# Performance work log

Hardware: AMD Instinct MI355X
Metric: run time of the kernel (lower is better)

The kernel has to match this reference:

```python
import jax, jax.numpy as jnp
import numpy as np

NUM_HEADS = 16
LN_EPS = 1e-5


def _layernorm(x, g, b):
    mu = jnp.mean(x, axis=-1, keepdims=True)
    var = jnp.mean(jnp.square(x - mu), axis=-1, keepdims=True)
    return (x - mu) * jax.lax.rsqrt(var + LN_EPS) * g + b


def setup_inputs() -> dict:
    key = jax.random.key(0)
    ks = jax.random.split(key, 8)
    B, S, D = 4, 2048, 1024
    s = 0.02  # small init so softmax/layernorm stay well-conditioned
    return {
        "x": jax.random.normal(ks[0], (B, S, D), jnp.float32),
        "wq_w": jax.random.normal(ks[1], (D, D), jnp.float32) * s,
        "wq_b": jnp.zeros((D,), jnp.float32),
        "wk_w": jax.random.normal(ks[2], (D, D), jnp.float32) * s,
        "wk_b": jnp.zeros((D,), jnp.float32),
        "wv_w": jax.random.normal(ks[3], (D, D), jnp.float32) * s,
        "wv_b": jnp.zeros((D,), jnp.float32),
        "ln1_g": jnp.ones((D,), jnp.float32),
        "ln1_b": jnp.zeros((D,), jnp.float32),
        "lin1_w": jax.random.normal(ks[4], (D, D), jnp.float32) * s,
        "lin1_b": jnp.zeros((D,), jnp.float32),
        "ln2_g": jnp.ones((D,), jnp.float32),
        "ln2_b": jnp.zeros((D,), jnp.float32),
    }


def reference(x, wq_w, wq_b, wk_w, wk_b, wv_w, wv_b,
              ln1_g, ln1_b, lin1_w, lin1_b, ln2_g, ln2_b):
    B, S, D = x.shape
    H = NUM_HEADS
    dh = D // H

    def proj(w, b):
        # torch Linear: x @ w.T + b ; split heads -> [B,H,S,dh]
        return (x @ w.T + b).reshape(B, S, H, dh).transpose(0, 2, 1, 3)

    q, k, v = proj(wq_w, wq_b), proj(wk_w, wk_b), proj(wv_w, wv_b)

    scores = jnp.einsum("bhqd,bhkd->bhqk", q, k) / jnp.sqrt(jnp.float32(dh))
    causal = jnp.tril(jnp.ones((S, S), jnp.bool_))  # True = attend
    scores = jnp.where(causal[None, None], scores, -jnp.inf)
    probs = jax.nn.softmax(scores, axis=-1)
    attn = jnp.einsum("bhqk,bhkd->bhqd", probs, v)
    attn = attn.transpose(0, 2, 1, 3).reshape(B, S, D)

    h = _layernorm(x + attn, ln1_g, ln1_b)
    h = _layernorm(h + (h @ lin1_w.T + lin1_b), ln2_g, ln2_b)
    return h
```

## Files before the change

### kernel.cpp

```cpp
#include <hip/hip_runtime.h>
#include <math.h>

#define B_  4
#define S_  2048
#define D_  1024
#define H_  16
#define DH_ 64
#define M_  (B_*S_)

typedef unsigned short ushort_t;
typedef __attribute__((ext_vector_type(8))) __bf16 bf16x8;
typedef __attribute__((ext_vector_type(4))) float f32x4;
typedef __attribute__((ext_vector_type(8))) unsigned short us8;
typedef __attribute__((ext_vector_type(4))) unsigned short us4;

__device__ __forceinline__ ushort_t f2bf(float f) {
    unsigned int u = __float_as_uint(f);
    u = (u + 0x7fffu + ((u >> 16) & 1u)) >> 16;
    return (ushort_t)u;
}
__device__ __forceinline__ float bf2f(ushort_t u) {
    return __uint_as_float(((unsigned int)u) << 16);
}

#define GLD16(gp, lp) __builtin_amdgcn_global_load_lds( \
    (const __attribute__((address_space(1))) void*)(gp), \
    (__attribute__((address_space(3))) void*)(lp), 16, 0, 0)

#define WAIT_VM0()   __builtin_amdgcn_s_waitcnt(0x0F70)
#define WAIT_VM4()   __builtin_amdgcn_s_waitcnt(0x0F74)
#define WAIT_VM8()   __builtin_amdgcn_s_waitcnt(0x0F78)
#define MEMFENCE()   asm volatile("" ::: "memory")
#define BAR()        do { MEMFENCE(); __builtin_amdgcn_s_barrier(); MEMFENCE(); } while (0)

__global__ __launch_bounds__(256)
void cvt_all(const float* __restrict__ x,
             const float* __restrict__ w0, const float* __restrict__ w1,
             const float* __restrict__ w2, const float* __restrict__ w3,
             ushort_t* __restrict__ xd, ushort_t* __restrict__ wd)
{
    const int bid = blockIdx.x;
    const float* s;
    ushort_t* d;
    int i;
    if (bid < 4096) {
        s = x; d = xd; i = bid * 2048 + threadIdx.x * 8;
    } else {
        const int k = (bid - 4096) >> 9;
        const int r = (bid - 4096) & 511;
        s = (k == 0) ? w0 : (k == 1) ? w1 : (k == 2) ? w2 : w3;
        d = wd + (size_t)k * (D_ * D_);
        i = r * 2048 + threadIdx.x * 8;
    }
    float4 a = *(const float4*)(s + i);
    float4 b = *(const float4*)(s + i + 4);
    us8 r8;
    r8[0] = f2bf(a.x); r8[1] = f2bf(a.y); r8[2] = f2bf(a.z); r8[3] = f2bf(a.w);
    r8[4] = f2bf(b.x); r8[5] = f2bf(b.y); r8[6] = f2bf(b.z); r8[7] = f2bf(b.w);
    *(us8*)(d + i) = r8;
}

__global__ __launch_bounds__(256)
void gemm_mfma(const ushort_t* __restrict__ A, const ushort_t* __restrict__ Bw,
               const float* __restrict__ bias0, const float* __restrict__ bias1,
               const float* __restrict__ bias2,
               ushort_t* __restrict__ Yb, ushort_t* __restrict__ Qo,
               ushort_t* __restrict__ Ko, ushort_t* __restrict__ Vo,
               int K, int mode)
{
    __shared__ __align__(16) ushort_t As[3][128 * 32];
    __shared__ __align__(16) ushort_t Bs[3][128 * 32];
    const int t = threadIdx.x;
    const int lane = t & 63, wave = t >> 6;
    const int wm = wave >> 1, wn = wave & 1;
    const int m0 = blockIdx.x * 128, n0 = blockIdx.y * 128;
    const int quad = lane >> 4, l15 = lane & 15;

    const int ch0 = wave * 2, ch1 = wave * 2 + 1;
    const int srow = lane >> 2;
    const int scol = 8 * ((lane & 3) ^ (srow & 3));
    const ushort_t* Ap0 = A  + (size_t)(m0 + ch0 * 16 + srow) * K + scol;
    const ushort_t* Ap1 = A  + (size_t)(m0 + ch1 * 16 + srow) * K + scol;
    const ushort_t* Bp0 = Bw + (size_t)(n0 + ch0 * 16 + srow) * K + scol;
    const ushort_t* Bp1 = Bw + (size_t)(n0 + ch1 * 16 + srow) * K + scol;

    f32x4 acc[4][4] = {};

    GLD16(Ap0, As[0] + ch0 * 512);
    GLD16(Ap1, As[0] + ch1 * 512);
    GLD16(Bp0, Bs[0] + ch0 * 512);
    GLD16(Bp1, Bs[0] + ch1 * 512);
    GLD16(Ap0 + 32, As[1] + ch0 * 512);
    GLD16(Ap1 + 32, As[1] + ch1 * 512);
    GLD16(Bp0 + 32, Bs[1] + ch0 * 512);
    GLD16(Bp1 + 32, Bs[1] + ch1 * 512);

    const int skq = 8 * (quad ^ (l15 & 3));

    const int nk = K >> 5;
    for (int ki = 0; ki < nk; ki++) {
        const int buf = ki % 3;
        if (ki + 2 < nk) {
            const int k2 = (ki + 2) << 5;
            const int b2 = (ki + 2) % 3;
            GLD16(Ap0 + k2, As[b2] + ch0 * 512);
            GLD16(Ap1 + k2, As[b2] + ch1 * 512);
            GLD16(Bp0 + k2, Bs[b2] + ch0 * 512);
            GLD16(Bp1 + k2, Bs[b2] + ch1 * 512);
            WAIT_VM8();
        } else if (ki + 1 < nk) {
            WAIT_VM4();
        } else {
            WAIT_VM0();
        }
        BAR();

        bf16x8 af[4], bfr[4];
        #pragma unroll
        for (int i = 0; i < 4; i++)
            af[i] = *(const bf16x8*)(As[buf] + (64 * wm + 16 * i + l15) * 32 + skq);
        #pragma unroll
        for (int j = 0; j < 4; j++)
            bfr[j] = *(const bf16x8*)(Bs[buf] + (64 * wn + 16 * j + l15) * 32 + skq);
        #pragma unroll
        for (int i = 0; i < 4; i++)
            #pragma unroll
            for (int j = 0; j < 4; j++)
                acc[i][j] = __builtin_amdgcn_mfma_f32_16x16x32_bf16(af[i], bfr[j], acc[i][j], 0, 0, 0);

        BAR();
    }

    #pragma unroll
    for (int j = 0; j < 4; j++) {
        const int n = n0 + 64 * wn + 16 * j + l15;
        if (mode == 1) {
            const float bv = bias0[n];
            #pragma unroll
            for (int i = 0; i < 4; i++) {
                const int mrow = m0 + 64 * wm + 16 * i + quad * 4;
                ushort_t* yp = Yb + (size_t)mrow * D_ + n;
                #pragma unroll
                for (int r = 0; r < 4; r++)
                    yp[(size_t)r * D_] = f2bf(acc[i][j][r] + bv);
            }
        } else {
            const int sel = n >> 10, nn = n & 1023;
            const int hh = nn >> 6, dd = nn & 63;
            const float bv = (sel == 0 ? bias0 : (sel == 1 ? bias1 : bias2))[nn];
            const float scl = (sel == 0) ? 0.18033688f : 1.0f;
            #pragma unroll
            for (int i = 0; i < 4; i++) {
                const int mrow = m0 + 64 * wm + 16 * i + quad * 4;
                const int b = mrow >> 11;
                const int ss = mrow & (S_ - 1);
                if (sel == 2) {
                    us4 pk;
                    #pragma unroll
                    for (int r = 0; r < 4; r++)
                        pk[r] = f2bf(acc[i][j][r] + bv);
                    *(us4*)(Vo + (((size_t)b * H_ + hh) * DH_ + dd) * S_ + ss) = pk;
                } else {
                    ushort_t* dst = (sel == 0) ? Qo : Ko;
                    #pragma unroll
                    for (int r = 0; r < 4; r++) {
                        const float v = (acc[i][j][r] + bv) * scl;
                        dst[(((size_t)b * H_ + hh) * S_ + ss + r) * DH_ + dd] = f2bf(v);
                    }
                }
            }
        }
    }
}

__global__ __launch_bounds__(256, 3)
void attn_mfma(const ushort_t* __restrict__ Qb, const ushort_t* __restrict__ Kb,
               const ushort_t* __restrict__ Vt, ushort_t* __restrict__ outb)
{
    __shared__ __align__(16) ushort_t Ks[2][64 * 64];
    __shared__ __align__(16) ushort_t Vs[2][64 * 64];
    __shared__ __align__(16) ushort_t Ps[8][16 * 72];
    const int t = threadIdx.x, lane = t & 63, w = t >> 6;
    const int bh = blockIdx.x;
    const int qt = 15 - (int)blockIdx.y;
    const int quad = lane >> 4, l15 = lane & 15;
    const int rw = 32 * w;

    const int c0 = 2 * w, c1 = 2 * w + 1;
    const int srow = lane >> 3;
    const int scol = 8 * ((lane & 7) ^ srow);
    const ushort_t* KgB = Kb + (size_t)bh * S_ * DH_;
    const ushort_t* VgB = Vt + (size_t)bh * DH_ * S_;
    const ushort_t* Kg0 = KgB + (size_t)(c0 * 8 + srow) * DH_ + scol;
    const ushort_t* Kg1 = KgB + (size_t)(c1 * 8 + srow) * DH_ + scol;
    const ushort_t* Vg0 = VgB + (size_t)(c0 * 8 + srow) * S_ + scol;
    const ushort_t* Vg1 = VgB + (size_t)(c1 * 8 + srow) * S_ + scol;
    ushort_t* pw0 = Ps[w * 2 + 0];
    ushort_t* pw1 = Ps[w * 2 + 1];
    const int b = bh >> 4, hh = bh & (H_ - 1);

    const int q0 = qt * 128;

    const ushort_t* qp = Qb + ((size_t)bh * S_ + q0 + rw + l15) * DH_ + quad * 8;
    const bf16x8 qf00 = *(const bf16x8*)(qp);
    const bf16x8 qf01 = *(const bf16x8*)(qp + 32);
    const bf16x8 qf10 = *(const bf16x8*)(qp + 16 * DH_);
    const bf16x8 qf11 = *(const bf16x8*)(qp + 16 * DH_ + 32);

    f32x4 o0[4] = {}, o1[4] = {};
    float la0 = 0.f, la1 = 0.f;

    WAIT_VM0();
    MEMFENCE();
    GLD16(Kg0, &Ks[0][c0 * 512]);
    GLD16(Kg1, &Ks[0][c1 * 512]);
    GLD16(Vg0, &Vs[0][c0 * 512]);
    GLD16(Vg1, &Vs[0][c1 * 512]);

    const int qg00 = q0 + rw;
    const int qg10 = q0 + rw + 16;
    const int last = 2 * qt + 1;

    for (int kt = 0; kt <= last; kt++) {
        const int buf = kt & 1;
        const int k0 = kt * 64;
        if (kt < last) {
            const size_t ko = (size_t)(k0 + 64) * DH_;
            GLD16(Kg0 + ko, &Ks[buf ^ 1][c0 * 512]);
            GLD16(Kg1 + ko, &Ks[buf ^ 1][c1 * 512]);
            GLD16(Vg0 + k0 + 64, &Vs[buf ^ 1][c0 * 512]);
            GLD16(Vg1 + k0 + 64, &Vs[buf ^ 1][c1 * 512]);
            WAIT_VM4();
        } else {
            WAIT_VM0();
        }
        BAR();

        if (k0 <= qg10 + 15) {
            const bool a0 = (k0 <= qg00 + 15);
            const ushort_t* kb = Ks[buf];
            const ushort_t* vb = Vs[buf];
            const int xr = l15 & 7;

            bf16x8 kf[4][2];
            #pragma unroll
            for (int ct = 0; ct < 4; ct++)
                #pragma unroll
                for (int h = 0; h < 2; h++)
                    kf[ct][h] = *(const bf16x8*)(kb + (ct * 16 + l15) * 64 +
                                                 8 * ((h * 4 + quad) ^ xr));

            const f32x4 cinit = { -16.f, -16.f, -16.f, -16.f };
            f32x4 sc0[4], sc1[4];
            #pragma unroll
            for (int ct = 0; ct < 4; ct++) { sc0[ct] = cinit; sc1[ct] = cinit; }
            __builtin_amdgcn_s_setprio(1);
            #pragma unroll
            for (int ct = 0; ct < 4; ct++) {
                sc1[ct] = __builtin_amdgcn_mfma_f32_16x16x32_bf16(kf[ct][0], qf10, sc1[ct], 0, 0, 0);
                sc1[ct] = __builtin_amdgcn_mfma_f32_16x16x32_bf16(kf[ct][1], qf11, sc1[ct], 0, 0, 0);
            }
            if (a0) {
                #pragma unroll
                for (int ct = 0; ct < 4; ct++) {
                    sc0[ct] = __builtin_amdgcn_mfma_f32_16x16x32_bf16(kf[ct][0], qf00, sc0[ct], 0, 0, 0);
                    sc0[ct] = __builtin_amdgcn_mfma_f32_16x16x32_bf16(kf[ct][1], qf01, sc0[ct], 0, 0, 0);
                }
            }
            __builtin_amdgcn_s_setprio(0);

            bf16x8 vf[4][2];
            #pragma unroll
            for (int mt = 0; mt < 4; mt++)
                #pragma unroll
                for (int h = 0; h < 2; h++)
                    vf[mt][h] = *(const bf16x8*)(vb + (mt * 16 + l15) * 64 +
                                                 8 * ((h * 4 + quad) ^ xr));

            if (k0 + 63 > qg10) {
                const int qq = qg10 + l15;
                #pragma unroll
                for (int ct = 0; ct < 4; ct++) {
                    const int key = k0 + ct * 16 + quad * 4;
                    #pragma unroll
                    for (int r = 0; r < 4; r++)
                        if (key + r > qq) sc1[ct][r] = -1e30f;
                }
            }
            if (a0 && k0 + 63 > qg00) {
                const int qq = qg00 + l15;
                #pragma unroll
                for (int ct = 0; ct < 4; ct++) {
                    const int key = k0 + ct * 16 + quad * 4;
                    #pragma unroll
                    for (int r = 0; r < 4; r++)
                        if (key + r > qq) sc0[ct][r] = -1e30f;
                }
            }

            #pragma unroll
            for (int ct = 0; ct < 4; ct++) {
                us4 pk;
                #pragma unroll
                for (int r = 0; r < 4; r++) {
                    const float p = exp2f(sc1[ct][r]);
                    la1 += p;
                    pk[r] = (ushort_t)(__float_as_uint(p) >> 16);
                }
                *(us4*)(pw1 + l15 * 72 + ct * 16 + quad * 4) = pk;
            }
            if (a0) {
                #pragma unroll
                for (int ct = 0; ct < 4; ct++) {
                    us4 pk;
                    #pragma unroll
                    for (int r = 0; r < 4; r++) {
                        const float p = exp2f(sc0[ct][r]);
                        la0 += p;
                        pk[r] = (ushort_t)(__float_as_uint(p) >> 16);
                    }
                    *(us4*)(pw0 + l15 * 72 + ct * 16 + quad * 4) = pk;
                }
            }

            __builtin_amdgcn_s_setprio(1);
            const bf16x8 pf10 = *(const bf16x8*)(pw1 + l15 * 72 + quad * 8);
            const bf16x8 pf11 = *(const bf16x8*)(pw1 + l15 * 72 + 32 + quad * 8);
            #pragma unroll
            for (int mt = 0; mt < 4; mt++) {
                o1[mt] = __builtin_amdgcn_mfma_f32_16x16x32_bf16(vf[mt][0], pf10, o1[mt], 0, 0, 0);
                o1[mt] = __builtin_amdgcn_mfma_f32_16x16x32_bf16(vf[mt][1], pf11, o1[mt], 0, 0, 0);
            }
            if (a0) {
                const bf16x8 pf00 = *(const bf16x8*)(pw0 + l15 * 72 + quad * 8);
                const bf16x8 pf01 = *(const bf16x8*)(pw0 + l15 * 72 + 32 + quad * 8);
                #pragma unroll
                for (int mt = 0; mt < 4; mt++) {
                    o0[mt] = __builtin_amdgcn_mfma_f32_16x16x32_bf16(vf[mt][0], pf00, o0[mt], 0, 0, 0);
                    o0[mt] = __builtin_amdgcn_mfma_f32_16x16x32_bf16(vf[mt][1], pf01, o0[mt], 0, 0, 0);
                }
            }
            __builtin_amdgcn_s_setprio(0);
        }
        BAR();
    }

    {
        la0 += __shfl_xor(la0, 16);
        la1 += __shfl_xor(la1, 16);
        la0 += __shfl_xor(la0, 32);
        la1 += __shfl_xor(la1, 32);
        const float inv0 = 1.0f / la0, inv1 = 1.0f / la1;
        const int query0 = q0 + rw + l15;
        ushort_t* ob0 = outb + ((size_t)(b * S_ + query0)) * D_ + hh * DH_ + quad * 4;
        ushort_t* ob1 = ob0 + (size_t)16 * D_;
        #pragma unroll
        for (int mt = 0; mt < 4; mt++) {
            us4 r0, r1;
            #pragma unroll
            for (int r = 0; r < 4; r++) {
                r0[r] = f2bf(o0[mt][r] * inv0);
                r1[r] = f2bf(o1[mt][r] * inv1);
            }
            *(us4*)(ob0 + mt * 16) = r0;
            *(us4*)(ob1 + mt * 16) = r1;
        }
    }
}

__global__ __launch_bounds__(256)
void ln_f32bf(const float* __restrict__ X, const ushort_t* __restrict__ R,
              const float* __restrict__ g, const float* __restrict__ bia,
              ushort_t* __restrict__ out_bf)
{
    const int row = blockIdx.x;
    const int t   = threadIdx.x;
    const float4 xv = ((const float4*)(X + (size_t)row * D_))[t];
    const us4 rv = *(const us4*)(R + (size_t)row * D_ + t * 4);
    float s0 = xv.x + bf2f(rv[0]);
    float s1 = xv.y + bf2f(rv[1]);
    float s2 = xv.z + bf2f(rv[2]);
    float s3 = xv.w + bf2f(rv[3]);

    float sum = s0 + s1 + s2 + s3;
    float sq  = s0*s0 + s1*s1 + s2*s2 + s3*s3;
    #pragma unroll
    for (int off = 32; off > 0; off >>= 1) {
        sum += __shfl_down(sum, off);
        sq  += __shfl_down(sq,  off);
    }
    __shared__ float wsum[4], wsq[4], stat[2];
    const int wid = t >> 6, lane = t & 63;
    if (lane == 0) { wsum[wid] = sum; wsq[wid] = sq; }
    __syncthreads();
    if (t == 0) {
        float S = wsum[0] + wsum[1] + wsum[2] + wsum[3];
        float Q = wsq[0]  + wsq[1]  + wsq[2]  + wsq[3];
        float mean = S * (1.0f / D_);
        float var  = Q * (1.0f / D_) - mean * mean;
        stat[0] = mean;
        stat[1] = rsqrtf(var + 1e-5f);
    }
    __syncthreads();
    const float mean = stat[0], inv = stat[1];
    const float4 gv = ((const float4*)g)[t];
    const float4 bv = ((const float4*)bia)[t];
    us4 ob;
    ob[0] = f2bf((s0 - mean) * inv * gv.x + bv.x);
    ob[1] = f2bf((s1 - mean) * inv * gv.y + bv.y);
    ob[2] = f2bf((s2 - mean) * inv * gv.z + bv.z);
    ob[3] = f2bf((s3 - mean) * inv * gv.w + bv.w);
    *(us4*)(out_bf + (size_t)row * D_ + t * 4) = ob;
}

__global__ __launch_bounds__(256)
void ln_bfbf(const ushort_t* __restrict__ Hb, const ushort_t* __restrict__ Yb,
             const float* __restrict__ g, const float* __restrict__ bia,
             float* __restrict__ outf)
{
    const int row = blockIdx.x;
    const int t   = threadIdx.x;
    const us4 hv = *(const us4*)(Hb + (size_t)row * D_ + t * 4);
    const us4 yv = *(const us4*)(Yb + (size_t)row * D_ + t * 4);
    float s0 = bf2f(hv[0]) + bf2f(yv[0]);
    float s1 = bf2f(hv[1]) + bf2f(yv[1]);
    float s2 = bf2f(hv[2]) + bf2f(yv[2]);
    float s3 = bf2f(hv[3]) + bf2f(yv[3]);

    float sum = s0 + s1 + s2 + s3;
    float sq  = s0*s0 + s1*s1 + s2*s2 + s3*s3;
    #pragma unroll
    for (int off = 32; off > 0; off >>= 1) {
        sum += __shfl_down(sum, off);
        sq  += __shfl_down(sq,  off);
    }
    __shared__ float wsum[4], wsq[4], stat[2];
    const int wid = t >> 6, lane = t & 63;
    if (lane == 0) { wsum[wid] = sum; wsq[wid] = sq; }
    __syncthreads();
    if (t == 0) {
        float S = wsum[0] + wsum[1] + wsum[2] + wsum[3];
        float Q = wsq[0]  + wsq[1]  + wsq[2]  + wsq[3];
        float mean = S * (1.0f / D_);
        float var  = Q * (1.0f / D_) - mean * mean;
        stat[0] = mean;
        stat[1] = rsqrtf(var + 1e-5f);
    }
    __syncthreads();
    const float mean = stat[0], inv = stat[1];
    const float4 gv = ((const float4*)g)[t];
    const float4 bv = ((const float4*)bia)[t];
    float4 o;
    o.x = (s0 - mean) * inv * gv.x + bv.x;
    o.y = (s1 - mean) * inv * gv.y + bv.y;
    o.z = (s2 - mean) * inv * gv.z + bv.z;
    o.w = (s3 - mean) * inv * gv.w + bv.w;
    ((float4*)(outf + (size_t)row * D_))[t] = o;
}

extern "C" void kernel_launch(void* const* d_in, const int* in_sizes, int n_in,
                              void* d_out, int out_size, void* d_ws, size_t ws_size,
                              hipStream_t stream)
{
    const float* x      = (const float*)d_in[0];
    const float* wq_w   = (const float*)d_in[1];
    const float* wq_b   = (const float*)d_in[2];
    const float* wk_w   = (const float*)d_in[3];
    const float* wk_b   = (const float*)d_in[4];
    const float* wv_w   = (const float*)d_in[5];
    const float* wv_b   = (const float*)d_in[6];
    const float* ln1_g  = (const float*)d_in[7];
    const float* ln1_b  = (const float*)d_in[8];
    const float* lin1_w = (const float*)d_in[9];
    const float* lin1_b = (const float*)d_in[10];
    const float* ln2_g  = (const float*)d_in[11];
    const float* ln2_b  = (const float*)d_in[12];
    float* out = (float*)d_out;

    char* base = (char*)d_ws;
    ushort_t* x_bf    = (ushort_t*)(base);
    ushort_t* attn_bf = (ushort_t*)(base);
    ushort_t* w_bf    = (ushort_t*)(base + 16777216);
    ushort_t* Qbf     = (ushort_t*)(base + 25165824);
    ushort_t* h_bf    = (ushort_t*)(base + 25165824);
    ushort_t* Kbf     = (ushort_t*)(base + 41943040);
    ushort_t* y_bf    = (ushort_t*)(base + 41943040);
    ushort_t* Vtp     = (ushort_t*)(base + 58720256);

    cvt_all<<<dim3(4096 + 4 * 512), 256, 0, stream>>>(
        x, wq_w, wk_w, wv_w, lin1_w, x_bf, w_bf);

    gemm_mfma<<<dim3(M_ / 128, 3072 / 128), 256, 0, stream>>>(
        x_bf, w_bf, wq_b, wk_b, wv_b, nullptr, Qbf, Kbf, Vtp, D_, 0);

    attn_mfma<<<dim3(64, 16), 256, 0, stream>>>(Qbf, Kbf, Vtp, attn_bf);

    ln_f32bf<<<M_, 256, 0, stream>>>(x, attn_bf, ln1_g, ln1_b, h_bf);

    gemm_mfma<<<dim3(M_ / 128, D_ / 128), 256, 0, stream>>>(
        h_bf, w_bf + 3 * D_ * D_, lin1_b, nullptr, nullptr, y_bf, nullptr, nullptr, nullptr, D_, 1);

    ln_bfbf<<<M_, 256, 0, stream>>>(h_bf, y_bf, ln2_g, ln2_b, out);
}
```

Measured before the change: 292.2 us.

## Single-buffer attention K/V via registers and use one wavefront per LayerNorm row

The attention kernel drops its double-buffered LDS K/V tiles and direct global-to-LDS loads. It now prefetches the next tile into registers during compute, then writes it to a single LDS buffer between two barriers, and raises the occupancy hint from 3 to 4 blocks per CU. The goal is to cut LDS use so more blocks fit per CU. The cost is an extra barrier per iteration and extra registers held for the prefetch. Both LayerNorm kernels now process four rows per block with one wavefront per row and shuffle-only reductions, which removes the shared-memory reductions and block syncs.

```diff
diff --git a/kernel.cpp b/kernel.cpp
--- a/kernel.cpp
+++ b/kernel.cpp
@@ -173,12 +173,12 @@
     }
 }
 
-__global__ __launch_bounds__(256, 3)
+__global__ __launch_bounds__(256, 4)
 void attn_mfma(const ushort_t* __restrict__ Qb, const ushort_t* __restrict__ Kb,
                const ushort_t* __restrict__ Vt, ushort_t* __restrict__ outb)
 {
-    __shared__ __align__(16) ushort_t Ks[2][64 * 64];
-    __shared__ __align__(16) ushort_t Vs[2][64 * 64];
+    __shared__ __align__(16) ushort_t Ks[64 * 64];
+    __shared__ __align__(16) ushort_t Vs[64 * 64];
     __shared__ __align__(16) ushort_t Ps[8][16 * 72];
     const int t = threadIdx.x, lane = t & 63, w = t >> 6;
     const int bh = blockIdx.x;
@@ -210,36 +210,39 @@
     f32x4 o0[4] = {}, o1[4] = {};
     float la0 = 0.f, la1 = 0.f;
 
-    WAIT_VM0();
-    MEMFENCE();
-    GLD16(Kg0, &Ks[0][c0 * 512]);
-    GLD16(Kg1, &Ks[0][c1 * 512]);
-    GLD16(Vg0, &Vs[0][c0 * 512]);
-    GLD16(Vg1, &Vs[0][c1 * 512]);
+    {
+        const us8 rk0 = *(const us8*)(Kg0);
+        const us8 rk1 = *(const us8*)(Kg1);
+        const us8 rv0 = *(const us8*)(Vg0);
+        const us8 rv1 = *(const us8*)(Vg1);
+        *(us8*)(Ks + c0 * 512 + lane * 8) = rk0;
+        *(us8*)(Ks + c1 * 512 + lane * 8) = rk1;
+        *(us8*)(Vs + c0 * 512 + lane * 8) = rv0;
+        *(us8*)(Vs + c1 * 512 + lane * 8) = rv1;
+    }
+    BAR();
 
     const int qg00 = q0 + rw;
     const int qg10 = q0 + rw + 16;
     const int last = 2 * qt + 1;
 
     for (int kt = 0; kt <= last; kt++) {
-        const int buf = kt & 1;
         const int k0 = kt * 64;
-        if (kt < last) {
+        const bool pre = (kt < last);
+
+        us8 nk0, nk1, nv0, nv1;
+        if (pre) {
             const size_t ko = (size_t)(k0 + 64) * DH_;
-            GLD16(Kg0 + ko, &Ks[buf ^ 1][c0 * 512]);
-            GLD16(Kg1 + ko, &Ks[buf ^ 1][c1 * 512]);
-            GLD16(Vg0 + k0 + 64, &Vs[buf ^ 1][c0 * 512]);
-            GLD16(Vg1 + k0 + 64, &Vs[buf ^ 1][c1 * 512]);
-            WAIT_VM4();
-        } else {
-            WAIT_VM0();
+            nk0 = *(const us8*)(Kg0 + ko);
+            nk1 = *(const us8*)(Kg1 + ko);
+            nv0 = *(const us8*)(Vg0 + k0 + 64);
+            nv1 = *(const us8*)(Vg1 + k0 + 64);
         }
-        BAR();
 
         if (k0 <= qg10 + 15) {
             const bool a0 = (k0 <= qg00 + 15);
-            const ushort_t* kb = Ks[buf];
-            const ushort_t* vb = Vs[buf];
+            const ushort_t* kb = Ks;
+            const ushort_t* vb = Vs;
             const int xr = l15 & 7;
 
             bf16x8 kf[4][2];
@@ -342,7 +345,15 @@
             }
             __builtin_amdgcn_s_setprio(0);
         }
-        BAR();
+
+        if (pre) {
+            BAR();
+            *(us8*)(Ks + c0 * 512 + lane * 8) = nk0;
+            *(us8*)(Ks + c1 * 512 + lane * 8) = nk1;
+            *(us8*)(Vs + c0 * 512 + lane * 8) = nv0;
+            *(us8*)(Vs + c1 * 512 + lane * 8) = nv1;
+            BAR();
+        }
     }
 
     {
@@ -373,44 +384,47 @@
               const float* __restrict__ g, const float* __restrict__ bia,
               ushort_t* __restrict__ out_bf)
 {
-    const int row = blockIdx.x;
-    const int t   = threadIdx.x;
-    const float4 xv = ((const float4*)(X + (size_t)row * D_))[t];
-    const us4 rv = *(const us4*)(R + (size_t)row * D_ + t * 4);
-    float s0 = xv.x + bf2f(rv[0]);
-    float s1 = xv.y + bf2f(rv[1]);
-    float s2 = xv.z + bf2f(rv[2]);
-    float s3 = xv.w + bf2f(rv[3]);
-
-    float sum = s0 + s1 + s2 + s3;
-    float sq  = s0*s0 + s1*s1 + s2*s2 + s3*s3;
-    #pragma unroll
-    for (int off = 32; off > 0; off >>= 1) {
-        sum += __shfl_down(sum, off);
-        sq  += __shfl_down(sq,  off);
-    }
-    __shared__ float wsum[4], wsq[4], stat[2];
-    const int wid = t >> 6, lane = t & 63;
-    if (lane == 0) { wsum[wid] = sum; wsq[wid] = sq; }
-    __syncthreads();
-    if (t == 0) {
-        float S = wsum[0] + wsum[1] + wsum[2] + wsum[3];
-        float Q = wsq[0]  + wsq[1]  + wsq[2]  + wsq[3];
-        float mean = S * (1.0f / D_);
-        float var  = Q * (1.0f / D_) - mean * mean;
-        stat[0] = mean;
-        stat[1] = rsqrtf(var + 1e-5f);
-    }
-    __syncthreads();
-    const float mean = stat[0], inv = stat[1];
-    const float4 gv = ((const float4*)g)[t];
-    const float4 bv = ((const float4*)bia)[t];
-    us4 ob;
-    ob[0] = f2bf((s0 - mean) * inv * gv.x + bv.x);
-    ob[1] = f2bf((s1 - mean) * inv * gv.y + bv.y);
-    ob[2] = f2bf((s2 - mean) * inv * gv.z + bv.z);
-    ob[3] = f2bf((s3 - mean) * inv * gv.w + bv.w);
-    *(us4*)(out_bf + (size_t)row * D_ + t * 4) = ob;
+    const int wid = threadIdx.x >> 6, lane = threadIdx.x & 63;
+    const int row = blockIdx.x * 4 + wid;
+    const float*   xr = X + (size_t)row * D_;
+    const ushort_t* rr = R + (size_t)row * D_;
+
+    float s[16];
+    float sum = 0.f, sq = 0.f;
+    #pragma unroll
+    for (int k = 0; k < 4; k++) {
+        const int off = k * 256 + lane * 4;
+        const float4 xv = *(const float4*)(xr + off);
+        const us4    rv = *(const us4*)(rr + off);
+        const float v0 = xv.x + bf2f(rv[0]);
+        const float v1 = xv.y + bf2f(rv[1]);
+        const float v2 = xv.z + bf2f(rv[2]);
+        const float v3 = xv.w + bf2f(rv[3]);
+        s[k*4+0] = v0; s[k*4+1] = v1; s[k*4+2] = v2; s[k*4+3] = v3;
+        sum += v0 + v1 + v2 + v3;
+        sq  += v0*v0 + v1*v1 + v2*v2 + v3*v3;
+    }
+    #pragma unroll
+    for (int off = 1; off < 64; off <<= 1) {
+        sum += __shfl_xor(sum, off);
+        sq  += __shfl_xor(sq,  off);
+    }
+    const float mean = sum * (1.0f / D_);
+    const float inv  = rsqrtf(sq * (1.0f / D_) - mean * mean + 1e-5f);
+
+    ushort_t* orow = out_bf + (size_t)row * D_;
+    #pragma unroll
+    for (int k = 0; k < 4; k++) {
+        const int off = k * 256 + lane * 4;
+        const float4 gv = *(const float4*)(g + off);
+        const float4 bv = *(const float4*)(bia + off);
+        us4 ob;
+        ob[0] = f2bf((s[k*4+0] - mean) * inv * gv.x + bv.x);
+        ob[1] = f2bf((s[k*4+1] - mean) * inv * gv.y + bv.y);
+        ob[2] = f2bf((s[k*4+2] - mean) * inv * gv.z + bv.z);
+        ob[3] = f2bf((s[k*4+3] - mean) * inv * gv.w + bv.w);
+        *(us4*)(orow + off) = ob;
+    }
 }
 
 __global__ __launch_bounds__(256)
@@ -418,44 +432,47 @@
              const float* __restrict__ g, const float* __restrict__ bia,
              float* __restrict__ outf)
 {
-    const int row = blockIdx.x;
-    const int t   = threadIdx.x;
-    const us4 hv = *(const us4*)(Hb + (size_t)row * D_ + t * 4);
-    const us4 yv = *(const us4*)(Yb + (size_t)row * D_ + t * 4);
-    float s0 = bf2f(hv[0]) + bf2f(yv[0]);
-    float s1 = bf2f(hv[1]) + bf2f(yv[1]);
-    float s2 = bf2f(hv[2]) + bf2f(yv[2]);
-    float s3 = bf2f(hv[3]) + bf2f(yv[3]);
-
-    float sum = s0 + s1 + s2 + s3;
-    float sq  = s0*s0 + s1*s1 + s2*s2 + s3*s3;
-    #pragma unroll
-    for (int off = 32; off > 0; off >>= 1) {
-        sum += __shfl_down(sum, off);
-        sq  += __shfl_down(sq,  off);
-    }
-    __shared__ float wsum[4], wsq[4], stat[2];
-    const int wid = t >> 6, lane = t & 63;
-    if (lane == 0) { wsum[wid] = sum; wsq[wid] = sq; }
-    __syncthreads();
-    if (t == 0) {
-        float S = wsum[0] + wsum[1] + wsum[2] + wsum[3];
-        float Q = wsq[0]  + wsq[1]  + wsq[2]  + wsq[3];
-        float mean = S * (1.0f / D_);
-        float var  = Q * (1.0f / D_) - mean * mean;
-        stat[0] = mean;
-        stat[1] = rsqrtf(var + 1e-5f);
-    }
-    __syncthreads();
-    const float mean = stat[0], inv = stat[1];
-    const float4 gv = ((const float4*)g)[t];
-    const float4 bv = ((const float4*)bia)[t];
-    float4 o;
-    o.x = (s0 - mean) * inv * gv.x + bv.x;
-    o.y = (s1 - mean) * inv * gv.y + bv.y;
-    o.z = (s2 - mean) * inv * gv.z + bv.z;
-    o.w = (s3 - mean) * inv * gv.w + bv.w;
-    ((float4*)(outf + (size_t)row * D_))[t] = o;
+    const int wid = threadIdx.x >> 6, lane = threadIdx.x & 63;
+    const int row = blockIdx.x * 4 + wid;
+    const ushort_t* hr = Hb + (size_t)row * D_;
+    const ushort_t* yr = Yb + (size_t)row * D_;
+
+    float s[16];
+    float sum = 0.f, sq = 0.f;
+    #pragma unroll
+    for (int k = 0; k < 4; k++) {
+        const int off = k * 256 + lane * 4;
+        const us4 hv = *(const us4*)(hr + off);
+        const us4 yv = *(const us4*)(yr + off);
+        const float v0 = bf2f(hv[0]) + bf2f(yv[0]);
+        const float v1 = bf2f(hv[1]) + bf2f(yv[1]);
+        const float v2 = bf2f(hv[2]) + bf2f(yv[2]);
+        const float v3 = bf2f(hv[3]) + bf2f(yv[3]);
+        s[k*4+0] = v0; s[k*4+1] = v1; s[k*4+2] = v2; s[k*4+3] = v3;
+        sum += v0 + v1 + v2 + v3;
+        sq  += v0*v0 + v1*v1 + v2*v2 + v3*v3;
+    }
+    #pragma unroll
+    for (int off = 1; off < 64; off <<= 1) {
+        sum += __shfl_xor(sum, off);
+        sq  += __shfl_xor(sq,  off);
+    }
+    const float mean = sum * (1.0f / D_);
+    const float inv  = rsqrtf(sq * (1.0f / D_) - mean * mean + 1e-5f);
+
+    float* orow = outf + (size_t)row * D_;
+    #pragma unroll
+    for (int k = 0; k < 4; k++) {
+        const int off = k * 256 + lane * 4;
+        const float4 gv = *(const float4*)(g + off);
+        const float4 bv = *(const float4*)(bia + off);
+        float4 o;
+        o.x = (s[k*4+0] - mean) * inv * gv.x + bv.x;
+        o.y = (s[k*4+1] - mean) * inv * gv.y + bv.y;
+        o.z = (s[k*4+2] - mean) * inv * gv.z + bv.z;
+        o.w = (s[k*4+3] - mean) * inv * gv.w + bv.w;
+        *(float4*)(orow + off) = o;
+    }
 }
 
 extern "C" void kernel_launch(void* const* d_in, const int* in_sizes, int n_in,
@@ -495,10 +512,10 @@
 
     attn_mfma<<<dim3(64, 16), 256, 0, stream>>>(Qbf, Kbf, Vtp, attn_bf);
 
-    ln_f32bf<<<M_, 256, 0, stream>>>(x, attn_bf, ln1_g, ln1_b, h_bf);
+    ln_f32bf<<<dim3(M_ / 4), 256, 0, stream>>>(x, attn_bf, ln1_g, ln1_b, h_bf);
 
     gemm_mfma<<<dim3(M_ / 128, D_ / 128), 256, 0, stream>>>(
         h_bf, w_bf + 3 * D_ * D_, lin1_b, nullptr, nullptr, y_bf, nullptr, nullptr, nullptr, D_, 1);
 
-    ln_bfbf<<<M_, 256, 0, stream>>>(h_bf, y_bf, ln2_g, ln2_b, out);
-}
+    ln_bfbf<<<dim3(M_ / 4), 256, 0, stream>>>(h_bf, y_bf, ln2_g, ln2_b, out);
+}
```

Measured after the change: 439.8 us. 50.5% more time.
